# Kernel tuning notes

Measured on AMD Instinct MI355X. Metric: run time of the kernel, lower is better.

## Reference

```python
import jax, jax.numpy as jnp
import numpy as np

EMB = 1024
HEADS = 16


def setup_inputs() -> dict:
    key = jax.random.key(0)
    ks = jax.random.split(key, 9)
    s = 1.0 / np.sqrt(EMB)
    x = jax.random.normal(ks[0], (2, 2048, EMB), dtype=jnp.float32)
    Wq = jax.random.normal(ks[1], (EMB, EMB), dtype=jnp.float32) * s
    bq = jnp.zeros((EMB,), dtype=jnp.float32)
    Wk = jax.random.normal(ks[2], (EMB, EMB), dtype=jnp.float32) * s
    bk = jnp.zeros((EMB,), dtype=jnp.float32)
    Wv = jax.random.normal(ks[3], (EMB, EMB), dtype=jnp.float32) * s
    bv = jnp.zeros((EMB,), dtype=jnp.float32)
    Wo = jax.random.normal(ks[4], (EMB, EMB), dtype=jnp.float32) * s
    bo = jnp.zeros((EMB,), dtype=jnp.float32)
    return {"x": x, "Wq": Wq, "bq": bq, "Wk": Wk, "bk": bk,
            "Wv": Wv, "bv": bv, "Wo": Wo, "bo": bo}


def reference(x, Wq, bq, Wk, bk, Wv, bv, Wo, bo):
    b, n, e = x.shape
    h = HEADS
    d = e // h
    # q/k/v projections -> [b, h, n, d]
    def split_heads(t):
        return t.reshape(b, n, h, d).transpose(0, 2, 1, 3)
    q = split_heads(x @ Wq.T + bq)
    k = split_heads(x @ Wk.T + bk)
    v = split_heads(x @ Wv.T + bv)
    # NOTE: original scales by sqrt(emb_size), not sqrt(head_dim)
    scaling = jnp.sqrt(jnp.float32(e))
    energy = jnp.einsum('bhqd,bhkd->bhqk', q, k)  # [b,h,n,n]
    att = jax.nn.softmax(energy / scaling, axis=-1)
    out = jnp.einsum('bhqk,bhkd->bhqd', att, v)
    out = out.transpose(0, 2, 1, 3).reshape(b, n, e)
    return out @ Wo.T + bo
```

## Files before the change

### kernel.cpp

```cpp
#include <hip/hip_runtime.h>


typedef short short8  __attribute__((ext_vector_type(8)));
typedef float floatx4 __attribute__((ext_vector_type(4)));

#define SEQ   2048
#define BATCH 2
#define NH    16
#define HD    64
#define EMB   1024

#define QSCALE 0.045084220027780106f

__device__ __forceinline__ unsigned short f32_bf16(float f) {
    unsigned int u = __float_as_uint(f);
    u += 0x7FFF + ((u >> 16) & 1);
    return (unsigned short)(u >> 16);
}

__device__ __forceinline__ unsigned int pk_bf16(float lo, float hi) {
    return __builtin_amdgcn_perm(__float_as_uint(hi) + 0x8000u,
                                 __float_as_uint(lo) + 0x8000u, 0x07060302u);
}

__device__ __forceinline__ void gl_lds16(const unsigned short* g,
                                         unsigned short* l) {
    __builtin_amdgcn_global_load_lds(
        (const __attribute__((address_space(1))) unsigned int*)g,
        (__attribute__((address_space(3))) unsigned int*)l, 16, 0, 0);
}

__global__ __launch_bounds__(256) void convert_all(
        const float* __restrict__ x,  const float* __restrict__ wq,
        const float* __restrict__ wk, const float* __restrict__ wv,
        const float* __restrict__ wo, unsigned short* __restrict__ dst) {
    int i = (blockIdx.x * 256 + threadIdx.x) * 4;
    const float* src; int off;
    if      (i < 4194304) { src = x;  off = 0; }
    else if (i < 5242880) { src = wq; off = 4194304; }
    else if (i < 6291456) { src = wk; off = 5242880; }
    else if (i < 7340032) { src = wv; off = 6291456; }
    else                  { src = wo; off = 7340032; }
    float4 v = *(const float4*)(src + (i - off));
    uint2 o;
    o.x = pk_bf16(v.x, v.y);
    o.y = pk_bf16(v.z, v.w);
    *(uint2*)(dst + i) = o;
}

template <int MODE>
__device__ __forceinline__ void gemm_bt_core(
        unsigned short (* __restrict__ sA)[64],
        unsigned short (* __restrict__ sB)[64],
        const unsigned short* __restrict__ A,
        const unsigned short* __restrict__ B,
        const float* __restrict__ bias,
        unsigned short* __restrict__ outb) {
    const int t    = threadIdx.x;
    const int wave = t >> 6, lane = t & 63;
    const int l15  = lane & 15, quad = lane >> 4;
    const int wm   = (wave >> 1) * 64, wn = (wave & 1) * 64;
    const int m0   = blockIdx.y * 128,  n0 = blockIdx.x * 128;
    const int srow = lane >> 3;
    const int sch  = ((lane & 7) ^ srow) * 8;

    floatx4 acc[4][4] = {};

    for (int k0 = 0; k0 < EMB; k0 += 64) {
        for (int i = 0; i < 4; ++i) {
            int rr  = wave * 32 + i * 8;
            int row = rr + srow;
            gl_lds16(&A[(size_t)(m0 + row) * EMB + k0 + sch], &sA[0][0] + rr * 64);
            gl_lds16(&B[(size_t)(n0 + row) * EMB + k0 + sch], &sB[0][0] + rr * 64);
        }
        __syncthreads();
        for (int ks = 0; ks < 2; ++ks) {
            const int ch = (((ks * 4) + quad) ^ (l15 & 7)) * 8;
            short8 af[4], bf[4];
            for (int i = 0; i < 4; ++i)
                af[i] = *(const short8*)&sA[wm + i * 16 + l15][ch];
            for (int j = 0; j < 4; ++j)
                bf[j] = *(const short8*)&sB[wn + j * 16 + l15][ch];
            for (int i = 0; i < 4; ++i)
                for (int j = 0; j < 4; ++j)
                    acc[i][j] = __builtin_amdgcn_mfma_f32_16x16x32_bf16(
                        af[i], bf[j], acc[i][j], 0, 0, 0);
        }
        __syncthreads();
    }
    if (MODE == 2) {
        for (int i = 0; i < 4; ++i) {
            int row = m0 + wm + i * 16 + quad * 4;
            int bb  = row >> 11, seq = row & 2047;
            for (int j = 0; j < 4; ++j) {
                int col = n0 + wn + j * 16 + l15;
                float bv = bias[col];
                int vtrow = (bb * 16 + (col >> 6)) * 64 + (col & 63);
                uint2 pk;
                pk.x = pk_bf16(acc[i][j][0] + bv, acc[i][j][1] + bv);
                pk.y = pk_bf16(acc[i][j][2] + bv, acc[i][j][3] + bv);
                *(uint2*)&outb[(size_t)vtrow * SEQ + seq] = pk;
            }
        }
    } else {
        const float sc2 = (MODE == 1) ? QSCALE : 1.0f;
        for (int i = 0; i < 4; ++i) {
            int row = m0 + wm + i * 16 + quad * 4;
            for (int j = 0; j < 4; ++j) {
                int col = n0 + wn + j * 16 + l15;
                float bv = bias[col];
                for (int r = 0; r < 4; ++r) {
                    float v = (acc[i][j][r] + bv) * sc2;
                    outb[(size_t)(row + r) * EMB + col] = f32_bf16(v);
                }
            }
        }
    }
}

__global__ __launch_bounds__(256, 3) void gemm_qkv(
        const unsigned short* __restrict__ xb,
        const unsigned short* __restrict__ wq,
        const unsigned short* __restrict__ wk,
        const unsigned short* __restrict__ wv,
        const float* __restrict__ bq, const float* __restrict__ bk,
        const float* __restrict__ bv,
        unsigned short* __restrict__ Q, unsigned short* __restrict__ K,
        unsigned short* __restrict__ VT) {
    __shared__ unsigned short sA[128][64];
    __shared__ unsigned short sB[128][64];
    if      (blockIdx.z == 0) gemm_bt_core<1>(sA, sB, xb, wq, bq, Q);
    else if (blockIdx.z == 1) gemm_bt_core<0>(sA, sB, xb, wk, bk, K);
    else                      gemm_bt_core<2>(sA, sB, xb, wv, bv, VT);
}

__global__ __launch_bounds__(256) void gemm_out(
        const unsigned short* __restrict__ A,
        const unsigned short* __restrict__ B,
        const float* __restrict__ bias, float* __restrict__ out) {
    __shared__ unsigned short sA[128][64];
    __shared__ unsigned short sB[64][64];
    const int t    = threadIdx.x;
    const int wave = t >> 6, lane = t & 63;
    const int l15  = lane & 15, quad = lane >> 4;
    const int wm   = wave * 32;
    const int m0   = blockIdx.y * 128,  n0 = blockIdx.x * 64;
    const int srow = lane >> 3;
    const int sch  = ((lane & 7) ^ srow) * 8;

    floatx4 acc[2][4] = {};

    for (int k0 = 0; k0 < EMB; k0 += 64) {
        {
            for (int i = 0; i < 4; ++i) {
                int rr = wave * 32 + i * 8;
                gl_lds16(&A[(size_t)(m0 + rr + srow) * EMB + k0 + sch],
                         &sA[0][0] + rr * 64);
            }
            for (int i = 0; i < 2; ++i) {
                int rr = wave * 16 + i * 8;
                gl_lds16(&B[(size_t)(n0 + rr + srow) * EMB + k0 + sch],
                         &sB[0][0] + rr * 64);
            }
        }
        __syncthreads();
        for (int ks = 0; ks < 2; ++ks) {
            const int ch = (((ks * 4) + quad) ^ (l15 & 7)) * 8;
            short8 af[2], bf[4];
            for (int i = 0; i < 2; ++i)
                af[i] = *(const short8*)&sA[wm + i * 16 + l15][ch];
            for (int j = 0; j < 4; ++j)
                bf[j] = *(const short8*)&sB[j * 16 + l15][ch];
            for (int i = 0; i < 2; ++i)
                for (int j = 0; j < 4; ++j)
                    acc[i][j] = __builtin_amdgcn_mfma_f32_16x16x32_bf16(
                        af[i], bf[j], acc[i][j], 0, 0, 0);
        }
        __syncthreads();
    }
    for (int i = 0; i < 2; ++i) {
        int row = m0 + wm + i * 16 + quad * 4;
        for (int j = 0; j < 4; ++j) {
            int col = n0 + j * 16 + l15;
            float bv = bias[col];
            for (int r = 0; r < 4; ++r)
                out[(size_t)(row + r) * EMB + col] = acc[i][j][r] + bv;
        }
    }
}

__global__ __launch_bounds__(512) void attn(
        const unsigned short* __restrict__ Q,
        const unsigned short* __restrict__ K,
        const unsigned short* __restrict__ VT,
        unsigned short* __restrict__ O) {
    __shared__ unsigned short sK [64][64];
    __shared__ unsigned short sVT[64][64];
    __shared__ unsigned short sP [128][72];
    const int t    = threadIdx.x;
    const int wave = t >> 6, lane = t & 63;
    const int l15  = lane & 15, quad = lane >> 4;
    const int bh   = blockIdx.x;
    const int b    = bh >> 4, h = bh & 15;
    const int q0   = blockIdx.y * 128;
    const size_t rowbase = (size_t)b * SEQ;
    const int colbase  = h * HD;
    const size_t vtbase = (size_t)bh * HD * SEQ;
    const int srow = lane >> 3;
    const int sch  = ((lane & 7) ^ srow) * 8;

    short8 qf[2];
    for (int ks = 0; ks < 2; ++ks)
        qf[ks] = *(const short8*)&Q[(rowbase + q0 + wave * 16 + l15) * EMB
                                    + colbase + ks * 32 + quad * 8];

    float l_part = 0.f;
    floatx4 o_acc[4] = {};

    for (int kt = 0; kt < SEQ; kt += 64) {
        {
            int rr  = wave * 8;
            int row = rr + srow;
            gl_lds16(&K[(rowbase + kt + row) * EMB + colbase + sch],
                     &sK[0][0] + rr * 64);
            gl_lds16(&VT[vtbase + (size_t)row * SEQ + kt + sch],
                     &sVT[0][0] + rr * 64);
        }
        __syncthreads();

        floatx4 s[4] = {};
        for (int ks = 0; ks < 2; ++ks) {
            const int ch = (((ks * 4) + quad) ^ (l15 & 7)) * 8;
            short8 kf[4];
            for (int mi = 0; mi < 4; ++mi)
                kf[mi] = *(const short8*)&sK[mi * 16 + l15][ch];
            for (int mi = 0; mi < 4; ++mi)
                s[mi] = __builtin_amdgcn_mfma_f32_16x16x32_bf16(
                    kf[mi], qf[ks], s[mi], 0, 0, 0);
        }

        {
            int prow = wave * 16 + l15;
            float lp = l_part;
            for (int mi = 0; mi < 4; ++mi) {
                float p0 = __builtin_amdgcn_exp2f(s[mi][0]);
                float p1 = __builtin_amdgcn_exp2f(s[mi][1]);
                float p2 = __builtin_amdgcn_exp2f(s[mi][2]);
                float p3 = __builtin_amdgcn_exp2f(s[mi][3]);
                lp += (p0 + p1) + (p2 + p3);
                uint2 pk;
                pk.x = pk_bf16(p0, p1);
                pk.y = pk_bf16(p2, p3);
                *(uint2*)&sP[prow][mi * 16 + quad * 4] = pk;
            }
            l_part = lp;
        }

        for (int ks = 0; ks < 2; ++ks) {
            const int ch = (((ks * 4) + quad) ^ (l15 & 7)) * 8;
            short8 vf[4];
            for (int mi = 0; mi < 4; ++mi)
                vf[mi] = *(const short8*)&sVT[mi * 16 + l15][ch];
            short8 pf = *(const short8*)&sP[wave * 16 + l15][ks * 32 + quad * 8];
            for (int mi = 0; mi < 4; ++mi)
                o_acc[mi] = __builtin_amdgcn_mfma_f32_16x16x32_bf16(
                    vf[mi], pf, o_acc[mi], 0, 0, 0);
        }
        __syncthreads();
    }

    float la = l_part;
    la += __shfl_xor(la, 16, 64);
    la += __shfl_xor(la, 32, 64);
    const float inv_l = 1.0f / la;

    {
        int prow = wave * 16 + l15;
        for (int mi = 0; mi < 4; ++mi) {
            uint2 pk;
            pk.x = pk_bf16(o_acc[mi][0] * inv_l, o_acc[mi][1] * inv_l);
            pk.y = pk_bf16(o_acc[mi][2] * inv_l, o_acc[mi][3] * inv_l);
            *(uint2*)&sP[prow][mi * 16 + quad * 4] = pk;
        }
    }
    __builtin_amdgcn_s_waitcnt(0);
    const int ql = lane >> 2, dh = (lane & 3) * 16;
    const size_t grow = rowbase + q0 + wave * 16 + ql;
    for (int i = 0; i < 2; ++i) {
        uint4 v = *(const uint4*)&sP[wave * 16 + ql][dh + i * 8];
        *(uint4*)&O[grow * EMB + colbase + dh + i * 8] = v;
    }
}

extern "C" void kernel_launch(void* const* d_in, const int* in_sizes, int n_in,
                              void* d_out, int out_size, void* d_ws, size_t ws_size,
                              hipStream_t stream) {
    const float* x  = (const float*)d_in[0];
    const float* Wq = (const float*)d_in[1];
    const float* bq = (const float*)d_in[2];
    const float* Wk = (const float*)d_in[3];
    const float* bk = (const float*)d_in[4];
    const float* Wv = (const float*)d_in[5];
    const float* bv = (const float*)d_in[6];
    const float* Wo = (const float*)d_in[7];
    const float* bo = (const float*)d_in[8];

    unsigned short* ws  = (unsigned short*)d_ws;
    unsigned short* xb  = ws;
    unsigned short* wqb = ws + 4194304;
    unsigned short* wkb = ws + 5242880;
    unsigned short* wvb = ws + 6291456;
    unsigned short* wob = ws + 7340032;
    unsigned short* Qb  = ws + 8388608;
    unsigned short* Kb  = ws + 12582912;
    unsigned short* VTb = ws + 16777216;
    unsigned short* Ob  = ws + 20971520;

    convert_all<<<8192, 256, 0, stream>>>(x, Wq, Wk, Wv, Wo, ws);
    gemm_qkv<<<dim3(8, 32, 3), 256, 0, stream>>>(xb, wqb, wkb, wvb,
                                                 bq, bk, bv, Qb, Kb, VTb);
    attn<<<dim3(32, 16), 512, 0, stream>>>(Qb, Kb, VTb, Ob);
    gemm_out<<<dim3(16, 32), 256, 0, stream>>>(Ob, wob, bo, (float*)d_out);
}
```

Measured before the change: 183.9 us.

## Triple-buffer K/V tiles in attention with async prefetch and one barrier

The attention kernel now keeps three LDS buffers for the K and V^T tiles. The next tile's global-to-LDS load is issued before the current tile is processed, and the wait uses explicit vmcnt counts followed by a raw s_barrier. The trailing __syncthreads per iteration is removed. This is meant to hide global load latency behind the MFMA and exp work and to halve barrier stalls. The cost is higher LDS use, which may reduce occupancy, and correctness now depends on the hand-written waitcnt and barrier ordering.

Result: no change. 184.2 us (+0.2%).

```diff
diff --git a/kernel.cpp b/kernel.cpp
--- a/kernel.cpp
+++ b/kernel.cpp
@@ -194,8 +194,8 @@
         const unsigned short* __restrict__ K,
         const unsigned short* __restrict__ VT,
         unsigned short* __restrict__ O) {
-    __shared__ unsigned short sK [64][64];
-    __shared__ unsigned short sVT[64][64];
+    __shared__ unsigned short sK [3][64][64];
+    __shared__ unsigned short sVT[3][64][64];
     __shared__ unsigned short sP [128][72];
     const int t    = threadIdx.x;
     const int wave = t >> 6, lane = t & 63;
@@ -217,23 +217,36 @@
     float l_part = 0.f;
     floatx4 o_acc[4] = {};
 
-    for (int kt = 0; kt < SEQ; kt += 64) {
-        {
-            int rr  = wave * 8;
-            int row = rr + srow;
+    const int rr  = wave * 8;
+    const int row = rr + srow;
+
+    gl_lds16(&K[(rowbase + row) * EMB + colbase + sch], &sK[0][0][0] + rr * 64);
+    gl_lds16(&VT[vtbase + (size_t)row * SEQ + sch],     &sVT[0][0][0] + rr * 64);
+
+    int cur = 0;
+    for (int it = 0; it < SEQ / 64; ++it) {
+        if (it < SEQ / 64 - 1) {
+            int nb = cur + 1; if (nb == 3) nb = 0;
+            int kt = (it + 1) * 64;
             gl_lds16(&K[(rowbase + kt + row) * EMB + colbase + sch],
-                     &sK[0][0] + rr * 64);
+                     &sK[nb][0][0] + rr * 64);
             gl_lds16(&VT[vtbase + (size_t)row * SEQ + kt + sch],
-                     &sVT[0][0] + rr * 64);
-        }
-        __syncthreads();
+                     &sVT[nb][0][0] + rr * 64);
+            asm volatile("s_waitcnt vmcnt(2)" ::: "memory");
+        } else {
+            asm volatile("s_waitcnt vmcnt(0)" ::: "memory");
+        }
+        asm volatile("s_barrier" ::: "memory");
+
+        const unsigned short (*cK)[64]  = sK[cur];
+        const unsigned short (*cVT)[64] = sVT[cur];
 
         floatx4 s[4] = {};
         for (int ks = 0; ks < 2; ++ks) {
             const int ch = (((ks * 4) + quad) ^ (l15 & 7)) * 8;
             short8 kf[4];
             for (int mi = 0; mi < 4; ++mi)
-                kf[mi] = *(const short8*)&sK[mi * 16 + l15][ch];
+                kf[mi] = *(const short8*)&cK[mi * 16 + l15][ch];
             for (int mi = 0; mi < 4; ++mi)
                 s[mi] = __builtin_amdgcn_mfma_f32_16x16x32_bf16(
                     kf[mi], qf[ks], s[mi], 0, 0, 0);
@@ -260,13 +273,13 @@
             const int ch = (((ks * 4) + quad) ^ (l15 & 7)) * 8;
             short8 vf[4];
             for (int mi = 0; mi < 4; ++mi)
-                vf[mi] = *(const short8*)&sVT[mi * 16 + l15][ch];
+                vf[mi] = *(const short8*)&cVT[mi * 16 + l15][ch];
             short8 pf = *(const short8*)&sP[wave * 16 + l15][ks * 32 + quad * 8];
             for (int mi = 0; mi < 4; ++mi)
                 o_acc[mi] = __builtin_amdgcn_mfma_f32_16x16x32_bf16(
                     vf[mi], pf, o_acc[mi], 0, 0, 0);
         }
-        __syncthreads();
+        cur = cur + 1; if (cur == 3) cur = 0;
     }
 
     float la = l_part;
```
